# Performance work log

Hardware: AMD Instinct MI355X
Metric: run time of the kernel (lower is better)

## Reference

```python
import jax, jax.numpy as jnp
import numpy as np

N, E, G = 20000, 640000, 64
D_IN, H, C, D_OUT = 256, 4, 64, 32
HC = H * C


def gat_layer(x, W, a_src, a_dst, b, src, dst, n_nodes, heads, ch):
    # x: [N, F_in], W: [F_in, H*C]
    h = (x @ W).reshape(n_nodes, heads, ch)          # [N,H,C]
    es = jnp.einsum('nhc,hc->nh', h, a_src)          # [N,H]
    ed = jnp.einsum('nhc,hc->nh', h, a_dst)
    e = jax.nn.leaky_relu(es[src] + ed[dst], 0.2)    # [Etot,H]
    m = jax.ops.segment_max(e, dst, num_segments=n_nodes)
    m = jnp.where(jnp.isfinite(m), m, 0.0)
    ex = jnp.exp(e - m[dst])
    denom = jax.ops.segment_sum(ex, dst, num_segments=n_nodes)
    alpha = ex / jnp.maximum(denom[dst], 1e-16)      # softmax over in-edges per dst
    out = jax.ops.segment_sum(alpha[:, :, None] * h[src], dst, num_segments=n_nodes)
    return out.reshape(n_nodes, heads * ch) + b


def setup_inputs() -> dict:
    key = jax.random.key(0)
    ks = jax.random.split(key, 14)
    g1 = 1.0 / np.sqrt(D_IN)
    g2 = 1.0 / np.sqrt(HC)
    inp = {
        'x': jax.random.normal(ks[0], (N, D_IN), jnp.float32),
        'edge_index': jax.random.randint(ks[1], (2, E), 0, N, jnp.int64 if jax.config.jax_enable_x64 else jnp.int32),
        'batch': jnp.sort(jax.random.randint(ks[2], (N,), 0, G)),
        'W1': jax.random.normal(ks[3], (D_IN, HC), jnp.float32) * g1,
        'a_src1': jax.random.normal(ks[4], (H, C), jnp.float32) * g2,
        'a_dst1': jax.random.normal(ks[5], (H, C), jnp.float32) * g2,
        'b1': jnp.zeros((HC,), jnp.float32),
        'W2': jax.random.normal(ks[6], (HC, HC), jnp.float32) * g2,
        'a_src2': jax.random.normal(ks[7], (H, C), jnp.float32) * g2,
        'a_dst2': jax.random.normal(ks[8], (H, C), jnp.float32) * g2,
        'b2': jnp.zeros((HC,), jnp.float32),
        'Wp': jax.random.normal(ks[9], (HC, D_OUT), jnp.float32) * g2,
        'bp': jnp.zeros((D_OUT,), jnp.float32),
    }
    return inp


def reference(x, edge_index, batch, W1, a_src1, a_dst1, b1, W2, a_src2, a_dst2, b2, Wp, bp):
    # add self-loops (PyG GATConv default)
    loop = jnp.arange(N, dtype=edge_index.dtype)
    src = jnp.concatenate([edge_index[0], loop])
    dst = jnp.concatenate([edge_index[1], loop])
    x1 = jax.nn.relu(gat_layer(x, W1, a_src1, a_dst1, b1, src, dst, N, H, C))
    # dropout p=0.6 is identity in eval mode
    x2 = jax.nn.relu(gat_layer(x1, W2, a_src2, a_dst2, b2, src, dst, N, H, C))
    node_scores = x2 @ Wp + bp                        # [N, D_OUT]
    sums = jax.ops.segment_sum(node_scores, batch, num_segments=G)
    counts = jax.ops.segment_sum(jnp.ones((N,), node_scores.dtype), batch, num_segments=G)
    return sums / jnp.maximum(counts, 1.0)[:, None]   # [G, D_OUT]
```

## Files before the change

### kernel.cpp

```cpp
#include <hip/hip_runtime.h>
#include <hip/hip_bf16.h>
#include <cstdint>

#define NNODES 20000
#define NEDGES 640000
#define ETOT   (NEDGES + NNODES)
#define NGROUP 64
#define HC     256
#define DOUT   32
#define EBLK   5120
#define NBLK   (NEDGES / EBLK)
#define CBLK   ((NNODES + 255) / 256)
#define GBLK   (NNODES / 16)
#define GPITCH 1280

typedef short bf16x8 __attribute__((ext_vector_type(8)));
typedef short s16x4  __attribute__((ext_vector_type(4)));
typedef float f32x4  __attribute__((ext_vector_type(4)));
typedef float f32x2  __attribute__((ext_vector_type(2)));
typedef int   s32x4  __attribute__((ext_vector_type(4)));
typedef unsigned int u32x4 __attribute__((ext_vector_type(4)));

__device__ __forceinline__ float b2f(__hip_bfloat16 v) { return __bfloat162float(v); }
__device__ __forceinline__ float bs2f(short v) {
    union { unsigned int u; float f; } c; c.u = ((unsigned int)(unsigned short)v) << 16; return c.f;
}
__device__ __forceinline__ short f2bs(float v) {
    __hip_bfloat16 b = __float2bfloat16(v);
    union { __hip_bfloat16 b; short s; } u; u.b = b; return u.s;
}
__device__ __forceinline__ float ldf(const void* __restrict__ p, size_t i, int bf) {
    return bf ? __bfloat162float(((const __hip_bfloat16*)p)[i]) : ((const float*)p)[i];
}
__device__ __forceinline__ int ld_idx(const int* __restrict__ p, size_t i, int f64) {
    return f64 ? p[2 * i] : p[i];
}
__device__ __forceinline__ int probe_edge64(const int* __restrict__ ei) {
    int l = threadIdx.x & 63;
    int zeros = 0;
#pragma unroll
    for (int r = 0; r < 4; r++)
        zeros += __popcll(__ballot(ei[2 * (r * 64 + l) + 1] == 0));
    return (zeros > 200) ? 1 : 0;
}
__device__ __forceinline__ int probe_xbf(const unsigned int* __restrict__ xw) {
    int l = threadIdx.x & 63;
    int ones = 0;
#pragma unroll
    for (int r = 0; r < 4; r++)
        ones += __popcll(__ballot((xw[r * 64 + l] >> 14) & 1));
    return (ones < 64) ? 1 : 0;
}

__global__ __launch_bounds__(256) void k_setup(const unsigned int* __restrict__ xw,
                                               const int* __restrict__ ei,
                                               const void* __restrict__ W1, const void* __restrict__ W2,
                                               __hip_bfloat16* __restrict__ Wt1,
                                               __hip_bfloat16* __restrict__ Wt2,
                                               int* __restrict__ H,
                                               float* __restrict__ sx, int* __restrict__ cnt,
                                               int* __restrict__ flag) {
    __shared__ int hl[NNODES];
    int t = threadIdx.x, b = blockIdx.x;
    if (b < NBLK) {
        int f = probe_edge64(ei);
        s32x4* hl4 = reinterpret_cast<s32x4*>(hl);
        for (int i = t; i < NNODES / 4; i += 256) hl4[i] = (s32x4){0, 0, 0, 0};
        __syncthreads();
        int s0 = b * EBLK;
        if (f) {
            const int* d64 = ei + 2 * NEDGES;
            for (int i0 = s0; i0 < s0 + EBLK; i0 += 512) {
                int i = i0 + 2 * t;
                s32x4 v = *reinterpret_cast<const s32x4*>(d64 + 2 * (size_t)i);
                atomicAdd(&hl[v[0]], 1);
                atomicAdd(&hl[v[2]], 1);
            }
        } else {
            const int* d32 = ei + NEDGES;
            for (int i0 = s0; i0 < s0 + EBLK; i0 += 1024) {
                int i = i0 + 4 * t;
                s32x4 v = *reinterpret_cast<const s32x4*>(d32 + i);
                atomicAdd(&hl[v[0]], 1); atomicAdd(&hl[v[1]], 1);
                atomicAdd(&hl[v[2]], 1); atomicAdd(&hl[v[3]], 1);
            }
        }
        __syncthreads();
        s32x4* Hb4 = reinterpret_cast<s32x4*>(H + (size_t)b * NNODES);
        for (int i = t; i < NNODES / 4; i += 256) Hb4[i] = hl4[i];
    } else {
        int bf = probe_xbf(xw);
        int i = (b - NBLK) * 256 + t;
        int which = i >> 16;
        int j = i & 65535;
        int k = j >> 8, n = j & 255;
        const void* W = which ? W2 : W1;
        __hip_bfloat16* Wt = which ? Wt2 : Wt1;
        Wt[(size_t)n * 256 + k] = __float2bfloat16(ldf(W, (size_t)k * 256 + n, bf));
        if (b == NBLK) {
            for (int q = t; q < NGROUP * HC; q += 256) sx[q] = 0.f;
            if (t < NGROUP) cnt[t] = 0;
            int f = probe_edge64(ei);
            if (t == 0) { flag[0] = f; flag[1] = bf; }
        }
    }
}

__global__ __launch_bounds__(256) void k_colsum(const int* __restrict__ H,
                                                int* __restrict__ deg,
                                                int* __restrict__ bsum) {
    __shared__ int wred[4];
    int t = threadIdx.x, n = blockIdx.x * 256 + t;
    int s = 0;
    if (n < NNODES) {
#pragma unroll 5
        for (int b = 0; b < NBLK; b++) s += H[(size_t)b * NNODES + n];
        s += 1;
        deg[n] = s;
    }
    int r = s;
#pragma unroll
    for (int o = 1; o < 64; o <<= 1) r += __shfl_xor(r, o);
    if ((t & 63) == 0) wred[t >> 6] = r;
    __syncthreads();
    if (t == 0) bsum[blockIdx.x] = wred[0] + wred[1] + wred[2] + wred[3];
}

__global__ __launch_bounds__(256) void k_base(int* __restrict__ H,
                                              const int* __restrict__ deg,
                                              const int* __restrict__ bsum,
                                              int* __restrict__ off,
                                              int* __restrict__ csr) {
    __shared__ int wtot[4];
    __shared__ int boff_s;
    int t = threadIdx.x, blk = blockIdx.x;
    int n = blk * 256 + t;
    int d = (n < NNODES) ? deg[n] : 0;
    int lane = t & 63, w = t >> 6;
    int sc = d;
#pragma unroll
    for (int o = 1; o < 64; o <<= 1) {
        int u = __shfl_up(sc, o);
        if (lane >= o) sc += u;
    }
    if (lane == 63) wtot[w] = sc;
    if (w == 0) {
        int v = (lane < blk) ? bsum[lane] : 0;
        if (lane + 64 < blk) v += bsum[lane + 64];
#pragma unroll
        for (int o = 1; o < 64; o <<= 1) v += __shfl_xor(v, o);
        if (lane == 0) boff_s = v;
    }
    __syncthreads();
    int woff = 0;
    for (int i = 0; i < w; i++) woff += wtot[i];
    int excl = woff + sc - d;
    if (blk == 0 && t == 0) off[NNODES] = ETOT;
    if (n < NNODES) {
        int o0 = boff_s + excl;
        off[n] = o0;
        csr[o0] = n;
        int run = o0 + 1;
#pragma unroll 5
        for (int b = 0; b < NBLK; b++) {
            size_t idx = (size_t)b * NNODES + n;
            int tt = H[idx];
            H[idx] = run;
            run += tt;
        }
    }
}

__global__ __launch_bounds__(256) void k_scatter2(const int* __restrict__ ei,
                                                  const int* __restrict__ H,
                                                  int* __restrict__ csr,
                                                  const int* __restrict__ flag) {
    __shared__ int base_l[NNODES];
    int t = threadIdx.x, b = blockIdx.x, f = flag[0];
    const s32x4* Hb4 = reinterpret_cast<const s32x4*>(H + (size_t)b * NNODES);
    s32x4* bl4 = reinterpret_cast<s32x4*>(base_l);
    for (int i = t; i < NNODES / 4; i += 256) bl4[i] = Hb4[i];
    __syncthreads();
    int s0 = b * EBLK;
    if (f) {
        const int* d64 = ei + 2 * NEDGES;
        for (int i0 = s0; i0 < s0 + EBLK; i0 += 512) {
            int i = i0 + 2 * t;
            s32x4 sv = *reinterpret_cast<const s32x4*>(ei + 2 * (size_t)i);
            s32x4 dv = *reinterpret_cast<const s32x4*>(d64 + 2 * (size_t)i);
            int p0 = atomicAdd(&base_l[dv[0]], 1);
            csr[p0] = sv[0];
            int p1 = atomicAdd(&base_l[dv[2]], 1);
            csr[p1] = sv[2];
        }
    } else {
        const int* d32 = ei + NEDGES;
        for (int i0 = s0; i0 < s0 + EBLK; i0 += 1024) {
            int i = i0 + 4 * t;
            s32x4 sv = *reinterpret_cast<const s32x4*>(ei + i);
            s32x4 dv = *reinterpret_cast<const s32x4*>(d32 + i);
#pragma unroll
            for (int k = 0; k < 4; k++) {
                int p = atomicAdd(&base_l[dv[k]], 1);
                csr[p] = sv[k];
            }
        }
    }
}

__global__ __launch_bounds__(256) void k_gemm(const void* __restrict__ A,
                                              const __hip_bfloat16* __restrict__ Bt,
                                              __hip_bfloat16* __restrict__ Hout,
                                              const void* __restrict__ a_src,
                                              const void* __restrict__ a_dst,
                                              float* __restrict__ es4, float* __restrict__ ed4,
                                              float* __restrict__ gpart,
                                              const int* __restrict__ flag, int force_bf) {
    __shared__ u32x4 hst4[512];
    int bf   = flag[1];
    int abf  = force_bf | bf;
    int w    = threadIdx.x >> 6;
    int lane = threadIdx.x & 63;
    int mr   = lane & 15;
    int quad = lane >> 4;
    int r0   = blockIdx.x * 16;
    f32x4 acc[4];
#pragma unroll
    for (int j = 0; j < 4; j++) acc[j] = (f32x4){0.f, 0.f, 0.f, 0.f};
    size_t rowoff = (size_t)(r0 + mr) * HC;
    const __hip_bfloat16* Btw = Bt + (size_t)w * 64 * HC;
    for (int kk = 0; kk < HC; kk += 32) {
        bf16x8 a;
        if (abf) {
            a = *reinterpret_cast<const bf16x8*>((const __hip_bfloat16*)A + rowoff + kk + quad * 8);
        } else {
            const float* af = (const float*)A + rowoff + kk + quad * 8;
            f32x4 lo = *reinterpret_cast<const f32x4*>(af);
            f32x4 hi = *reinterpret_cast<const f32x4*>(af + 4);
#pragma unroll
            for (int ii = 0; ii < 4; ii++) { a[ii] = f2bs(lo[ii]); a[ii + 4] = f2bs(hi[ii]); }
        }
#pragma unroll
        for (int j = 0; j < 4; j++) {
            bf16x8 b = *reinterpret_cast<const bf16x8*>(Btw + (size_t)(j * 16 + mr) * HC + kk + quad * 8);
            acc[j] = __builtin_amdgcn_mfma_f32_16x16x32_bf16(a, b, acc[j], 0, 0, 0);
        }
    }
    short* hst = reinterpret_cast<short*>(hst4);
#pragma unroll
    for (int j = 0; j < 4; j++)
#pragma unroll
        for (int r = 0; r < 4; r++)
            hst[(quad * 4 + r) * HC + w * 64 + j * 16 + mr] = f2bs(acc[j][r]);
    float ps[4] = {0.f, 0.f, 0.f, 0.f}, pd[4] = {0.f, 0.f, 0.f, 0.f};
#pragma unroll
    for (int j = 0; j < 4; j++) {
        float asv = ldf(a_src, (size_t)(w * 64 + j * 16 + mr), bf);
        float adv = ldf(a_dst, (size_t)(w * 64 + j * 16 + mr), bf);
#pragma unroll
        for (int r = 0; r < 4; r++) {
            ps[r] = fmaf(acc[j][r], asv, ps[r]);
            pd[r] = fmaf(acc[j][r], adv, pd[r]);
        }
    }
#pragma unroll
    for (int o = 1; o < 16; o <<= 1)
#pragma unroll
        for (int r = 0; r < 4; r++) {
            ps[r] += __shfl_xor(ps[r], o);
            pd[r] += __shfl_xor(pd[r], o);
        }
    float pm = fmaxf(fmaxf(ps[0], ps[1]), fmaxf(ps[2], ps[3]));
    pm = fmaxf(pm, __shfl_xor(pm, 16));
    pm = fmaxf(pm, __shfl_xor(pm, 32));
    if (lane == 0) gpart[w * GPITCH + blockIdx.x] = pm;
    if (mr == 0)
#pragma unroll
        for (int r = 0; r < 4; r++) {
            int row = r0 + quad * 4 + r;
            es4[(size_t)row * 4 + w] = ps[r];
            ed4[(size_t)row * 4 + w] = pd[r];
        }
    __syncthreads();
    u32x4* dst = reinterpret_cast<u32x4*>((short*)Hout + (size_t)r0 * HC);
    dst[threadIdx.x]       = hst4[threadIdx.x];
    dst[threadIdx.x + 256] = hst4[threadIdx.x + 256];
}

__global__ __launch_bounds__(256) void k_agg(const __hip_bfloat16* __restrict__ Hb,
                                             const float* __restrict__ es4, const float* __restrict__ ed4,
                                             const void* __restrict__ bias,
                                             const int* __restrict__ off, const int* __restrict__ csr,
                                             const float* __restrict__ gpart,
                                             const int* __restrict__ flag,
                                             __hip_bfloat16* __restrict__ out) {
    __shared__ float p_lds[4][4][64];
    __shared__ int   s_lds[4][64];
    __shared__ float gm_lds[4];
    int wv = threadIdx.x >> 6;
    int l  = threadIdx.x & 63;
    int half = l >> 5;
    int hl   = l & 31;
    int hd8  = hl >> 3;
    int bf = flag[1];
    {
        float m = -INFINITY;
        for (int i = l; i < GBLK; i += 64) m = fmaxf(m, gpart[wv * GPITCH + i]);
#pragma unroll
        for (int o = 32; o; o >>= 1) m = fmaxf(m, __shfl_xor(m, o));
        if (l == 0) gm_lds[wv] = m;
    }
    __syncthreads();
    f32x4 gm = (f32x4){gm_lds[0], gm_lds[1], gm_lds[2], gm_lds[3]};
    int n0 = blockIdx.x * 4 + wv;
    for (int n = n0; n < NNODES; n += 10000) {
        int base = off[n], deg = off[n + 1] - base;
        f32x4 edv = *reinterpret_cast<const f32x4*>(ed4 + (size_t)n * 4);
        f32x4 M;
#pragma unroll
        for (int h = 0; h < 4; h++) {
            float t0 = gm[h] + edv[h];
            M[h] = (t0 > 0.f) ? t0 : 0.2f * t0;
        }
        f32x4 dsum = (f32x4){0.f, 0.f, 0.f, 0.f};
        f32x2 acc2[4];
#pragma unroll
        for (int d = 0; d < 4; d++) acc2[d] = (f32x2){0.f, 0.f};
        for (int c0 = 0; c0 < deg; c0 += 64) {
            int cn = min(deg - c0, 64);
            int s = 0;
            f32x4 pv = (f32x4){0.f, 0.f, 0.f, 0.f};
            if (l < cn) {
                s = csr[base + c0 + l];
                f32x4 e = *reinterpret_cast<const f32x4*>(es4 + (size_t)s * 4);
#pragma unroll
                for (int h = 0; h < 4; h++) {
                    float t = e[h] + edv[h];
                    t = (t > 0.f) ? t : 0.2f * t;
                    pv[h] = __expf(t - M[h]);
                }
            }
            s_lds[wv][l] = s;
#pragma unroll
            for (int h = 0; h < 4; h++) p_lds[wv][h][l] = pv[h];
#pragma unroll
            for (int h = 0; h < 4; h++) dsum[h] += pv[h];
            int jn = (cn + 15) & ~15;
            for (int j = 0; j < jn; j += 16) {
                int e0 = j + 8 * half;
                s32x4 sA = *reinterpret_cast<const s32x4*>(&s_lds[wv][e0]);
                s32x4 sB = *reinterpret_cast<const s32x4*>(&s_lds[wv][e0 + 4]);
                f32x4 pA = *reinterpret_cast<const f32x4*>(&p_lds[wv][hd8][e0]);
                f32x4 pB = *reinterpret_cast<const f32x4*>(&p_lds[wv][hd8][e0 + 4]);
                u32x4 hv[8];
#pragma unroll
                for (int i = 0; i < 8; i++) {
                    int sj = (i < 4) ? sA[i & 3] : sB[i & 3];
                    hv[i] = *reinterpret_cast<const u32x4*>(Hb + (size_t)sj * HC + hl * 8);
                }
#pragma unroll
                for (int i = 0; i < 8; i++) {
                    float p = (i < 4) ? pA[i & 3] : pB[i & 3];
#pragma unroll
                    for (int d = 0; d < 4; d++) {
                        unsigned int u = hv[i][d];
                        f32x2 h2;
                        h2.x = __uint_as_float(u << 16);
                        h2.y = __uint_as_float(u & 0xFFFF0000u);
                        acc2[d] += h2 * p;
                    }
                }
            }
        }
#pragma unroll
        for (int o = 32; o; o >>= 1)
#pragma unroll
            for (int h = 0; h < 4; h++) dsum[h] += __shfl_xor(dsum[h], o);
#pragma unroll
        for (int d = 0; d < 4; d++) {
            acc2[d].x += __shfl_xor(acc2[d].x, 32);
            acc2[d].y += __shfl_xor(acc2[d].y, 32);
        }
        float rinv = 1.0f / fmaxf(dsum[hd8], 1e-16f);
        if (half == 0) {
            bf16x8 ov;
#pragma unroll
            for (int d = 0; d < 4; d++) {
                float v0 = acc2[d].x * rinv + ldf(bias, (size_t)hl * 8 + 2 * d, bf);
                float v1 = acc2[d].y * rinv + ldf(bias, (size_t)hl * 8 + 2 * d + 1, bf);
                ov[2 * d]     = f2bs(fmaxf(v0, 0.f));
                ov[2 * d + 1] = f2bs(fmaxf(v1, 0.f));
            }
            *reinterpret_cast<bf16x8*>(out + (size_t)n * HC + hl * 8) = ov;
        }
    }
}

__global__ __launch_bounds__(256) void k_groupsum(const __hip_bfloat16* __restrict__ X2,
                                                  const int* __restrict__ batch,
                                                  float* __restrict__ sx, int* __restrict__ cnt,
                                                  const int* __restrict__ flag) {
    const int RPB = NNODES / 250;
    int b = blockIdx.x, f = flag[0];
    int sub = threadIdx.x >> 6, l = threadIdx.x & 63;
    int r = b * RPB + sub;
    f32x4 acc = (f32x4){0.f, 0.f, 0.f, 0.f};
    int curg = ld_idx(batch, r, f);
    int cacc = 0;
    for (int k = 0; k < RPB / 4; k++, r += 4) {
        int g = ld_idx(batch, r, f);
        if (g != curg) {
#pragma unroll
            for (int c = 0; c < 4; c++) atomicAdd(&sx[(size_t)curg * HC + l * 4 + c], acc[c]);
            if (l == 0) atomicAdd(&cnt[curg], cacc);
            acc = (f32x4){0.f, 0.f, 0.f, 0.f}; cacc = 0; curg = g;
        }
        s16x4 hv = *reinterpret_cast<const s16x4*>(X2 + (size_t)r * HC + l * 4);
#pragma unroll
        for (int c = 0; c < 4; c++) acc[c] += bs2f(hv[c]);
        cacc++;
    }
#pragma unroll
    for (int c = 0; c < 4; c++) atomicAdd(&sx[(size_t)curg * HC + l * 4 + c], acc[c]);
    if (l == 0) atomicAdd(&cnt[curg], cacc);
}

__global__ __launch_bounds__(256) void k_final(const float* __restrict__ sx,
                                               const void* __restrict__ Wp,
                                               const void* __restrict__ bp,
                                               const int* __restrict__ cnt,
                                               const int* __restrict__ flag,
                                               void* __restrict__ out) {
    __shared__ float red[8][32];
    int g = blockIdx.x, t = threadIdx.x;
    int c = t & 31, seg = t >> 5;
    int bf = flag[1];
    const float* sxg = sx + (size_t)g * HC;
    float a = 0.f;
#pragma unroll
    for (int k = 0; k < 32; k++) {
        int kk = seg * 32 + k;
        a = fmaf(sxg[kk], ldf(Wp, (size_t)kk * DOUT + c, bf), a);
    }
    red[seg][c] = a;
    __syncthreads();
    if (t < 32) {
        float s = 0.f;
#pragma unroll
        for (int i = 0; i < 8; i++) s += red[i][t];
        int ct = cnt[g];
        float v = (ct > 0) ? (s / ct + ldf(bp, (size_t)t, bf)) : 0.f;
        if (bf) ((__hip_bfloat16*)out)[g * DOUT + t] = __float2bfloat16(v);
        else    ((float*)out)[g * DOUT + t]          = v;
    }
}

extern "C" void kernel_launch(void* const* d_in, const int* in_sizes, int n_in,
                              void* d_out, int out_size, void* d_ws, size_t ws_size,
                              hipStream_t stream) {
    (void)in_sizes; (void)n_in; (void)out_size; (void)ws_size;
    const void* x   = d_in[0];
    const int*  ei  = (const int*)d_in[1];
    const int*  bat = (const int*)d_in[2];
    const void* W1  = d_in[3];
    const void* as1 = d_in[4];
    const void* ad1 = d_in[5];
    const void* b1  = d_in[6];
    const void* W2  = d_in[7];
    const void* as2 = d_in[8];
    const void* ad2 = d_in[9];
    const void* b2  = d_in[10];
    const void* Wp  = d_in[11];
    const void* bp  = d_in[12];

    char* ws = (char*)d_ws;
    size_t o = 0;
    auto alloc = [&](size_t bytes) -> char* {
        char* p = ws + o;
        o += (bytes + 255) & ~(size_t)255;
        return p;
    };
    __hip_bfloat16* hb  = (__hip_bfloat16*)alloc((size_t)NNODES * HC * 2);
    __hip_bfloat16* xb  = (__hip_bfloat16*)alloc((size_t)NNODES * HC * 2);
    __hip_bfloat16* xb2 = (__hip_bfloat16*)alloc((size_t)NNODES * HC * 2);
    __hip_bfloat16* Wt1 = (__hip_bfloat16*)alloc((size_t)HC * HC * 2);
    __hip_bfloat16* Wt2 = (__hip_bfloat16*)alloc((size_t)HC * HC * 2);
    float* es = (float*)alloc((size_t)NNODES * 4 * 4);
    float* ed = (float*)alloc((size_t)NNODES * 4 * 4);
    int* H    = (int*)alloc((size_t)NBLK * NNODES * 4);
    int* deg  = (int*)alloc((size_t)NNODES * 4);
    int* off  = (int*)alloc((size_t)(NNODES + 1) * 4);
    int* csr  = (int*)alloc((size_t)ETOT * 4);
    int* bsum = (int*)alloc((size_t)CBLK * 4);
    float* gpart = (float*)alloc((size_t)4 * GPITCH * 4);
    float* sx = (float*)alloc((size_t)NGROUP * HC * 4);
    int* cnt  = (int*)alloc(256);
    int* flag = (int*)alloc(256);

    k_setup<<<NBLK + 512, 256, 0, stream>>>((const unsigned int*)x, ei, W1, W2,
                                            Wt1, Wt2, H, sx, cnt, flag);
    k_colsum<<<CBLK, 256, 0, stream>>>(H, deg, bsum);
    k_base<<<CBLK, 256, 0, stream>>>(H, deg, bsum, off, csr);
    k_scatter2<<<NBLK, 256, 0, stream>>>(ei, H, csr, flag);

    k_gemm<<<GBLK, 256, 0, stream>>>(x, Wt1, hb, as1, ad1, es, ed, gpart, flag, 0);
    k_agg<<<2500, 256, 0, stream>>>(hb, es, ed, b1, off, csr, gpart, flag, xb);

    k_gemm<<<GBLK, 256, 0, stream>>>(xb, Wt2, hb, as2, ad2, es, ed, gpart, flag, 1);
    k_agg<<<2500, 256, 0, stream>>>(hb, es, ed, b2, off, csr, gpart, flag, xb2);

    k_groupsum<<<250, 256, 0, stream>>>(xb2, bat, sx, cnt, flag);
    k_final<<<NGROUP, 256, 0, stream>>>(sx, Wp, bp, cnt, flag, d_out);
}
```

Before: 307.9 us.

## Co-schedule CSR scatter with layer-1 GEMM and replace partial-max array with atomics

Measured after the change: 300.4 us. -2.4%, faster.

```diff
diff --git a/kernel.cpp b/kernel.cpp
--- a/kernel.cpp
+++ b/kernel.cpp
@@ -12,7 +12,7 @@
 #define NBLK   (NEDGES / EBLK)
 #define CBLK   ((NNODES + 255) / 256)
 #define GBLK   (NNODES / 16)
-#define GPITCH 1280
+#define HALFN  10240
 
 typedef short bf16x8 __attribute__((ext_vector_type(8)));
 typedef short s16x4  __attribute__((ext_vector_type(4)));
@@ -21,7 +21,6 @@
 typedef int   s32x4  __attribute__((ext_vector_type(4)));
 typedef unsigned int u32x4 __attribute__((ext_vector_type(4)));
 
-__device__ __forceinline__ float b2f(__hip_bfloat16 v) { return __bfloat162float(v); }
 __device__ __forceinline__ float bs2f(short v) {
     union { unsigned int u; float f; } c; c.u = ((unsigned int)(unsigned short)v) << 16; return c.f;
 }
@@ -35,6 +34,13 @@
 __device__ __forceinline__ int ld_idx(const int* __restrict__ p, size_t i, int f64) {
     return f64 ? p[2 * i] : p[i];
 }
+__device__ __forceinline__ unsigned enc_f(float f) {
+    unsigned u = __float_as_uint(f);
+    return (u >> 31) ? ~u : (u | 0x80000000u);
+}
+__device__ __forceinline__ float dec_f(unsigned e) {
+    return (e >> 31) ? __uint_as_float(e & 0x7FFFFFFFu) : __uint_as_float(~e);
+}
 __device__ __forceinline__ int probe_edge64(const int* __restrict__ ei) {
     int l = threadIdx.x & 63;
     int zeros = 0;
@@ -54,12 +60,13 @@
 
 __global__ __launch_bounds__(256) void k_setup(const unsigned int* __restrict__ xw,
                                                const int* __restrict__ ei,
+                                               const int* __restrict__ bat,
                                                const void* __restrict__ W1, const void* __restrict__ W2,
                                                __hip_bfloat16* __restrict__ Wt1,
                                                __hip_bfloat16* __restrict__ Wt2,
                                                int* __restrict__ H,
                                                float* __restrict__ sx, int* __restrict__ cnt,
-                                               int* __restrict__ flag) {
+                                               unsigned* __restrict__ gp2) {
     __shared__ int hl[NNODES];
     int t = threadIdx.x, b = blockIdx.x;
     if (b < NBLK) {
@@ -99,9 +106,13 @@
         Wt[(size_t)n * 256 + k] = __float2bfloat16(ldf(W, (size_t)k * 256 + n, bf));
         if (b == NBLK) {
             for (int q = t; q < NGROUP * HC; q += 256) sx[q] = 0.f;
-            if (t < NGROUP) cnt[t] = 0;
+            if (t < 256) gp2[t] = 0x007FFFFFu;
             int f = probe_edge64(ei);
-            if (t == 0) { flag[0] = f; flag[1] = bf; }
+            if (t < NGROUP) hl[t] = 0;
+            __syncthreads();
+            for (int r = t; r < NNODES; r += 256) atomicAdd(&hl[ld_idx(bat, r, f)], 1);
+            __syncthreads();
+            if (t < NGROUP) cnt[t] = hl[t];
         }
     }
 }
@@ -171,59 +182,56 @@
     }
 }
 
-__global__ __launch_bounds__(256) void k_scatter2(const int* __restrict__ ei,
-                                                  const int* __restrict__ H,
-                                                  int* __restrict__ csr,
-                                                  const int* __restrict__ flag) {
-    __shared__ int base_l[NNODES];
-    int t = threadIdx.x, b = blockIdx.x, f = flag[0];
-    const s32x4* Hb4 = reinterpret_cast<const s32x4*>(H + (size_t)b * NNODES);
-    s32x4* bl4 = reinterpret_cast<s32x4*>(base_l);
-    for (int i = t; i < NNODES / 4; i += 256) bl4[i] = Hb4[i];
-    __syncthreads();
-    int s0 = b * EBLK;
-    if (f) {
-        const int* d64 = ei + 2 * NEDGES;
-        for (int i0 = s0; i0 < s0 + EBLK; i0 += 512) {
-            int i = i0 + 2 * t;
-            s32x4 sv = *reinterpret_cast<const s32x4*>(ei + 2 * (size_t)i);
-            s32x4 dv = *reinterpret_cast<const s32x4*>(d64 + 2 * (size_t)i);
-            int p0 = atomicAdd(&base_l[dv[0]], 1);
-            csr[p0] = sv[0];
-            int p1 = atomicAdd(&base_l[dv[2]], 1);
-            csr[p1] = sv[2];
-        }
-    } else {
-        const int* d32 = ei + NEDGES;
-        for (int i0 = s0; i0 < s0 + EBLK; i0 += 1024) {
-            int i = i0 + 4 * t;
-            s32x4 sv = *reinterpret_cast<const s32x4*>(ei + i);
-            s32x4 dv = *reinterpret_cast<const s32x4*>(d32 + i);
-#pragma unroll
-            for (int k = 0; k < 4; k++) {
-                int p = atomicAdd(&base_l[dv[k]], 1);
-                csr[p] = sv[k];
-            }
-        }
-    }
-}
-
-__global__ __launch_bounds__(256) void k_gemm(const void* __restrict__ A,
-                                              const __hip_bfloat16* __restrict__ Bt,
-                                              __hip_bfloat16* __restrict__ Hout,
-                                              const void* __restrict__ a_src,
-                                              const void* __restrict__ a_dst,
-                                              float* __restrict__ es4, float* __restrict__ ed4,
-                                              float* __restrict__ gpart,
-                                              const int* __restrict__ flag, int force_bf) {
-    __shared__ u32x4 hst4[512];
-    int bf   = flag[1];
-    int abf  = force_bf | bf;
+__device__ __forceinline__ void dev_scatter(int b, int f, const int* __restrict__ ei,
+                                            const int* __restrict__ H, int* __restrict__ csr,
+                                            int* hl) {
+    int t = threadIdx.x;
+    for (int pass = 0; pass < 2; ++pass) {
+        int nbase = pass * HALFN;
+        int span = NNODES - nbase; if (span > HALFN) span = HALFN;
+        const int* Hb = H + (size_t)b * NNODES + nbase;
+        for (int i = t; i < span; i += 256) hl[i] = Hb[i];
+        __syncthreads();
+        int s0 = b * EBLK;
+        if (f) {
+            const int* d64 = ei + 2 * NEDGES;
+            for (int i0 = s0; i0 < s0 + EBLK; i0 += 512) {
+                int i = i0 + 2 * t;
+                s32x4 sv = *reinterpret_cast<const s32x4*>(ei + 2 * (size_t)i);
+                s32x4 dv = *reinterpret_cast<const s32x4*>(d64 + 2 * (size_t)i);
+                unsigned d0 = (unsigned)(dv[0] - nbase), d1 = (unsigned)(dv[2] - nbase);
+                if (d0 < (unsigned)span) { int p = atomicAdd(&hl[d0], 1); csr[p] = sv[0]; }
+                if (d1 < (unsigned)span) { int p = atomicAdd(&hl[d1], 1); csr[p] = sv[2]; }
+            }
+        } else {
+            const int* d32 = ei + NEDGES;
+            for (int i0 = s0; i0 < s0 + EBLK; i0 += 1024) {
+                int i = i0 + 4 * t;
+                s32x4 sv = *reinterpret_cast<const s32x4*>(ei + i);
+                s32x4 dv = *reinterpret_cast<const s32x4*>(d32 + i);
+#pragma unroll
+                for (int k = 0; k < 4; k++) {
+                    unsigned d = (unsigned)(dv[k] - nbase);
+                    if (d < (unsigned)span) { int p = atomicAdd(&hl[d], 1); csr[p] = sv[k]; }
+                }
+            }
+        }
+        if (pass == 0) __syncthreads();
+    }
+}
+
+__device__ __forceinline__ void dev_gemm(int tile, const void* __restrict__ A,
+                                         const __hip_bfloat16* __restrict__ Bt,
+                                         __hip_bfloat16* __restrict__ Hout,
+                                         const void* __restrict__ a_src, const void* __restrict__ a_dst,
+                                         float* __restrict__ es4, float* __restrict__ ed4,
+                                         unsigned* __restrict__ gp2, int bf, int abf,
+                                         u32x4* hst4) {
     int w    = threadIdx.x >> 6;
     int lane = threadIdx.x & 63;
     int mr   = lane & 15;
     int quad = lane >> 4;
-    int r0   = blockIdx.x * 16;
+    int r0   = tile * 16;
     f32x4 acc[4];
 #pragma unroll
     for (int j = 0; j < 4; j++) acc[j] = (f32x4){0.f, 0.f, 0.f, 0.f};
@@ -273,7 +281,7 @@
     float pm = fmaxf(fmaxf(ps[0], ps[1]), fmaxf(ps[2], ps[3]));
     pm = fmaxf(pm, __shfl_xor(pm, 16));
     pm = fmaxf(pm, __shfl_xor(pm, 32));
-    if (lane == 0) gpart[w * GPITCH + blockIdx.x] = pm;
+    if (lane == 0) atomicMax(&gp2[w * 64 + (tile & 63)], enc_f(pm));
     if (mr == 0)
 #pragma unroll
         for (int r = 0; r < 4; r++) {
@@ -287,31 +295,61 @@
     dst[threadIdx.x + 256] = hst4[threadIdx.x + 256];
 }
 
-__global__ __launch_bounds__(256) void k_agg(const __hip_bfloat16* __restrict__ Hb,
+__global__ __launch_bounds__(256) void k_sg1(const void* __restrict__ x,
+                                             const int* __restrict__ ei,
+                                             const int* __restrict__ H, int* __restrict__ csr,
+                                             const __hip_bfloat16* __restrict__ Wt1,
+                                             __hip_bfloat16* __restrict__ hb,
+                                             const void* __restrict__ as1, const void* __restrict__ ad1,
+                                             float* __restrict__ es, float* __restrict__ ed,
+                                             unsigned* __restrict__ gp2) {
+    __shared__ int smem[HALFN];
+    int b = blockIdx.x;
+    if (b < NBLK) {
+        int f = probe_edge64(ei);
+        dev_scatter(b, f, ei, H, csr, smem);
+    } else {
+        int bf = probe_xbf((const unsigned int*)x);
+        dev_gemm(b - NBLK, x, Wt1, hb, as1, ad1, es, ed, gp2, bf, bf, (u32x4*)smem);
+    }
+}
+
+__global__ __launch_bounds__(256) void k_gemm2(const void* __restrict__ x,
+                                               const __hip_bfloat16* __restrict__ xb,
+                                               const __hip_bfloat16* __restrict__ Wt2,
+                                               __hip_bfloat16* __restrict__ hb,
+                                               const void* __restrict__ as2, const void* __restrict__ ad2,
+                                               float* __restrict__ es, float* __restrict__ ed,
+                                               unsigned* __restrict__ gp2) {
+    __shared__ u32x4 hst4[512];
+    int bf = probe_xbf((const unsigned int*)x);
+    dev_gemm(blockIdx.x, xb, Wt2, hb, as2, ad2, es, ed, gp2, bf, 1, hst4);
+}
+
+__global__ __launch_bounds__(256) void k_agg(const void* __restrict__ x,
+                                             const __hip_bfloat16* __restrict__ Hb,
                                              const float* __restrict__ es4, const float* __restrict__ ed4,
                                              const void* __restrict__ bias,
                                              const int* __restrict__ off, const int* __restrict__ csr,
-                                             const float* __restrict__ gpart,
-                                             const int* __restrict__ flag,
+                                             const unsigned* __restrict__ gp2,
                                              __hip_bfloat16* __restrict__ out) {
     __shared__ float p_lds[4][4][64];
     __shared__ int   s_lds[4][64];
-    __shared__ float gm_lds[4];
+    __shared__ float gm_s[4];
     int wv = threadIdx.x >> 6;
     int l  = threadIdx.x & 63;
     int half = l >> 5;
     int hl   = l & 31;
     int hd8  = hl >> 3;
-    int bf = flag[1];
+    int bf = probe_xbf((const unsigned int*)x);
     {
-        float m = -INFINITY;
-        for (int i = l; i < GBLK; i += 64) m = fmaxf(m, gpart[wv * GPITCH + i]);
+        float m = dec_f(gp2[wv * 64 + l]);
 #pragma unroll
         for (int o = 32; o; o >>= 1) m = fmaxf(m, __shfl_xor(m, o));
-        if (l == 0) gm_lds[wv] = m;
+        if (l == 0) gm_s[wv] = m;
     }
     __syncthreads();
-    f32x4 gm = (f32x4){gm_lds[0], gm_lds[1], gm_lds[2], gm_lds[3]};
+    f32x4 gm = (f32x4){gm_s[0], gm_s[1], gm_s[2], gm_s[3]};
     int n0 = blockIdx.x * 4 + wv;
     for (int n = n0; n < NNODES; n += 10000) {
         int base = off[n], deg = off[n + 1] - base;
@@ -396,45 +434,42 @@
     }
 }
 
-__global__ __launch_bounds__(256) void k_groupsum(const __hip_bfloat16* __restrict__ X2,
+__global__ __launch_bounds__(256) void k_groupsum(const int* __restrict__ ei,
+                                                  const __hip_bfloat16* __restrict__ X2,
                                                   const int* __restrict__ batch,
-                                                  float* __restrict__ sx, int* __restrict__ cnt,
-                                                  const int* __restrict__ flag) {
+                                                  float* __restrict__ sx) {
     const int RPB = NNODES / 250;
-    int b = blockIdx.x, f = flag[0];
+    int b = blockIdx.x;
+    int f = probe_edge64(ei);
     int sub = threadIdx.x >> 6, l = threadIdx.x & 63;
     int r = b * RPB + sub;
     f32x4 acc = (f32x4){0.f, 0.f, 0.f, 0.f};
     int curg = ld_idx(batch, r, f);
-    int cacc = 0;
     for (int k = 0; k < RPB / 4; k++, r += 4) {
         int g = ld_idx(batch, r, f);
         if (g != curg) {
 #pragma unroll
             for (int c = 0; c < 4; c++) atomicAdd(&sx[(size_t)curg * HC + l * 4 + c], acc[c]);
-            if (l == 0) atomicAdd(&cnt[curg], cacc);
-            acc = (f32x4){0.f, 0.f, 0.f, 0.f}; cacc = 0; curg = g;
+            acc = (f32x4){0.f, 0.f, 0.f, 0.f}; curg = g;
         }
         s16x4 hv = *reinterpret_cast<const s16x4*>(X2 + (size_t)r * HC + l * 4);
 #pragma unroll
         for (int c = 0; c < 4; c++) acc[c] += bs2f(hv[c]);
-        cacc++;
     }
 #pragma unroll
     for (int c = 0; c < 4; c++) atomicAdd(&sx[(size_t)curg * HC + l * 4 + c], acc[c]);
-    if (l == 0) atomicAdd(&cnt[curg], cacc);
-}
-
-__global__ __launch_bounds__(256) void k_final(const float* __restrict__ sx,
+}
+
+__global__ __launch_bounds__(256) void k_final(const void* __restrict__ x,
+                                               const float* __restrict__ sx,
                                                const void* __restrict__ Wp,
                                                const void* __restrict__ bp,
                                                const int* __restrict__ cnt,
-                                               const int* __restrict__ flag,
                                                void* __restrict__ out) {
     __shared__ float red[8][32];
     int g = blockIdx.x, t = threadIdx.x;
     int c = t & 31, seg = t >> 5;
-    int bf = flag[1];
+    int bf = probe_xbf((const unsigned int*)x);
     const float* sxg = sx + (size_t)g * HC;
     float a = 0.f;
 #pragma unroll
@@ -492,23 +527,18 @@
     int* off  = (int*)alloc((size_t)(NNODES + 1) * 4);
     int* csr  = (int*)alloc((size_t)ETOT * 4);
     int* bsum = (int*)alloc((size_t)CBLK * 4);
-    float* gpart = (float*)alloc((size_t)4 * GPITCH * 4);
+    unsigned* gp2 = (unsigned*)alloc(256 * 4);
     float* sx = (float*)alloc((size_t)NGROUP * HC * 4);
     int* cnt  = (int*)alloc(256);
-    int* flag = (int*)alloc(256);
-
-    k_setup<<<NBLK + 512, 256, 0, stream>>>((const unsigned int*)x, ei, W1, W2,
-                                            Wt1, Wt2, H, sx, cnt, flag);
+
+    k_setup<<<NBLK + 512, 256, 0, stream>>>((const unsigned int*)x, ei, bat, W1, W2,
+                                            Wt1, Wt2, H, sx, cnt, gp2);
     k_colsum<<<CBLK, 256, 0, stream>>>(H, deg, bsum);
     k_base<<<CBLK, 256, 0, stream>>>(H, deg, bsum, off, csr);
-    k_scatter2<<<NBLK, 256, 0, stream>>>(ei, H, csr, flag);
-
-    k_gemm<<<GBLK, 256, 0, stream>>>(x, Wt1, hb, as1, ad1, es, ed, gpart, flag, 0);
-    k_agg<<<2500, 256, 0, stream>>>(hb, es, ed, b1, off, csr, gpart, flag, xb);
-
-    k_gemm<<<GBLK, 256, 0, stream>>>(xb, Wt2, hb, as2, ad2, es, ed, gpart, flag, 1);
-    k_agg<<<2500, 256, 0, stream>>>(hb, es, ed, b2, off, csr, gpart, flag, xb2);
-
-    k_groupsum<<<250, 256, 0, stream>>>(xb2, bat, sx, cnt, flag);
-    k_final<<<NGROUP, 256, 0, stream>>>(sx, Wp, bp, cnt, flag, d_out);
-}
+    k_sg1<<<NBLK + GBLK, 256, 0, stream>>>(x, ei, H, csr, Wt1, hb, as1, ad1, es, ed, gp2);
+    k_agg<<<2500, 256, 0, stream>>>(x, hb, es, ed, b1, off, csr, gp2, xb);
+    k_gemm2<<<GBLK, 256, 0, stream>>>(x, xb, Wt2, hb, as2, ad2, es, ed, gp2);
+    k_agg<<<2500, 256, 0, stream>>>(x, hb, es, ed, b2, off, csr, gp2, xb2);
+    k_groupsum<<<250, 256, 0, stream>>>(ei, xb2, bat, sx);
+    k_final<<<NGROUP, 256, 0, stream>>>(x, sx, Wp, bp, cnt, d_out);
+}
```
